# Performance work log

Hardware: AMD Instinct MI355X
Metric: run time of the kernel (lower is better)

## Reference

```python
import jax, jax.numpy as jnp
import numpy as np

H = 256   # input_size
P = 256   # state_size
BATCH, L = 8, 4096
DT_MIN, DT_MAX = 1e-3, 1e-1
LN_EPS = 1e-5


def _hippo_params():
    # HiPPO-N matrix (num_blocks=1), eigendecomposition in numpy (float64 then cast)
    idx = np.arange(P, dtype=np.float64)
    s = np.sqrt(idx + 0.5)
    A = -np.outer(s, s)
    A = np.tril(A) - np.triu(A, 1)
    np.fill_diagonal(A, -0.5)
    ev, V = np.linalg.eig(A)
    order = np.argsort(ev.real)
    ev, V = ev[order], V[:, order]
    return ev, V


def setup_inputs() -> dict:
    key = jax.random.key(0)
    k_u, = jax.random.split(key, 1)
    ev, V = _hippo_params()
    rng = np.random.default_rng(0)
    log_lambda_real = np.log(-np.clip(ev.real, None, -1e-4)).astype(np.float32)
    lambda_imag = ev.imag.astype(np.float32)
    V_inv = np.linalg.inv(V)
    B_init = rng.standard_normal((P, H)) / np.sqrt(P)
    B_tilde = V_inv @ B_init.astype(np.complex128)
    C_init = rng.standard_normal((H, P)) / np.sqrt(P)
    C_tilde = C_init.astype(np.complex128) @ V
    log_delta = (rng.random(P) * (np.log(DT_MAX) - np.log(DT_MIN)) + np.log(DT_MIN)).astype(np.float32)
    return {
        "u": jax.random.normal(k_u, (BATCH, L, H), dtype=jnp.float32),
        "log_lambda_real": jnp.asarray(log_lambda_real),
        "lambda_imag": jnp.asarray(lambda_imag),
        "B_tilde_real": jnp.asarray(B_tilde.real, dtype=jnp.float32),
        "B_tilde_imag": jnp.asarray(B_tilde.imag, dtype=jnp.float32),
        "C_tilde_real": jnp.asarray(C_tilde.real, dtype=jnp.float32),
        "C_tilde_imag": jnp.asarray(C_tilde.imag, dtype=jnp.float32),
        "log_delta": jnp.asarray(log_delta),
        "gamma": jnp.ones((H,), dtype=jnp.float32),
        "beta": jnp.zeros((H,), dtype=jnp.float32),
    }


def _layernorm(x, gamma, beta):
    mu = jnp.mean(x, axis=-1, keepdims=True)
    var = jnp.mean(jnp.square(x - mu), axis=-1, keepdims=True)
    return (x - mu) * jax.lax.rsqrt(var + LN_EPS) * gamma + beta


def _ssm(h, log_lambda_real, lambda_imag, B_tilde_real, B_tilde_imag,
         C_tilde_real, C_tilde_imag, log_delta):
    # Continuous-time diagonal SSM params
    lam = -jnp.exp(log_lambda_real) + 1j * lambda_imag            # (P,) complex
    B_tilde = B_tilde_real + 1j * B_tilde_imag                     # (P,H)
    C_tilde = C_tilde_real + 1j * C_tilde_imag                     # (H,P)
    delta = jnp.exp(log_delta)                                     # (P,)
    # ZOH discretization (eq. 6 of the S5 paper)
    lambda_bar = jnp.exp(lam * delta)                              # (P,)
    B_bar = ((lambda_bar - 1.0) / lam)[:, None] * B_tilde          # (P,H)
    # Bu_k = B_bar @ u_k  ->  (B,L,P) complex
    Bu = jnp.einsum('blh,ph->blp', h.astype(jnp.complex64), B_bar.astype(jnp.complex64))
    # Parallel associative scan for x_k = lambda_bar * x_{k-1} + Bu_k
    a = jnp.broadcast_to(lambda_bar.astype(jnp.complex64), Bu.shape)
    def combine(c1, c2):
        a1, b1 = c1
        a2, b2 = c2
        return a1 * a2, a2 * b1 + b2
    _, xs = jax.lax.associative_scan(combine, (a, Bu), axis=1)     # (B,L,P)
    # Project back to real output: y = Re(C_tilde @ x)
    y = jnp.einsum('blp,hp->blh', xs, C_tilde.astype(jnp.complex64)).real
    return y


def reference(u, log_lambda_real, lambda_imag, B_tilde_real, B_tilde_imag,
              C_tilde_real, C_tilde_imag, log_delta, gamma, beta):
    # S5Block: pre-LayerNorm -> S5 SSM -> GELU -> residual
    h = _layernorm(u, gamma, beta)
    y = _ssm(h, log_lambda_real, lambda_imag, B_tilde_real, B_tilde_imag,
             C_tilde_real, C_tilde_imag, log_delta)
    return u + jax.nn.gelu(y)
```

## Files before the change

### kernel.cpp

```cpp
#include <hip/hip_runtime.h>
#include <math.h>

#define HDIM 256
#define PDIM 256
#define BATCH 8
#define LSEQ 4096
#define MTOT (BATCH * LSEQ)
#define NCHUNK 128
#define CHLEN 32

typedef __attribute__((ext_vector_type(8))) short bf16x8;
typedef __attribute__((ext_vector_type(4))) float f32x4;

__device__ __forceinline__ unsigned short f2bf(float f) {
    union { float f; unsigned int u; } v; v.f = f;
    unsigned int r = v.u + 0x7FFFu + ((v.u >> 16) & 1u);
    return (unsigned short)(r >> 16);
}
__device__ __forceinline__ float bf2f(unsigned int lo16) {
    union { unsigned int u; float f; } v; v.u = lo16 << 16;
    return v.f;
}

__device__ __forceinline__ void gload_lds16(const void* g, void* l) {
    __builtin_amdgcn_global_load_lds(
        (const __attribute__((address_space(1))) void*)g,
        (__attribute__((address_space(3))) void*)l, 16, 0, 0);
}

__global__ void wpack_k(const float* __restrict__ llr, const float* __restrict__ lim,
                        const float* __restrict__ ldl,
                        const float* __restrict__ Br, const float* __restrict__ Bi,
                        const float* __restrict__ Cr, const float* __restrict__ Ci,
                        unsigned short* __restrict__ W1t, unsigned short* __restrict__ W2t,
                        float* __restrict__ par) {
    int h = threadIdx.x;
    if (blockIdx.x < PDIM) {
        int p = blockIdx.x;
        float er = expf(llr[p]);
        float im = lim[p];
        float d  = expf(ldl[p]);
        float zr = -er * d, zi = im * d;
        float ea = expf(zr);
        float sz, cz; sincosf(zi, &sz, &cz);
        float ar = ea * cz, ai = ea * sz;
        float dr = -er, di = im;
        float den = dr * dr + di * di;
        float nr = ar - 1.0f, ni = ai;
        float cr = (nr * dr + ni * di) / den;
        float ci = (ni * dr - nr * di) / den;
        float br = Br[p * HDIM + h], bi = Bi[p * HDIM + h];
        W1t[(2 * p) * HDIM + h]     = f2bf(cr * br - ci * bi);
        W1t[(2 * p + 1) * HDIM + h] = f2bf(cr * bi + ci * br);
    } else if (blockIdx.x < 2 * PDIM) {
        int p = blockIdx.x - PDIM;
        W2t[h * (2 * PDIM) + 2 * p]     = f2bf(Cr[h * PDIM + p]);
        W2t[h * (2 * PDIM) + 2 * p + 1] = f2bf(-Ci[h * PDIM + p]);
    } else {
        int p = h;
        float er = expf(llr[p]);
        float im = lim[p];
        float d  = expf(ldl[p]);
        float zr = -er * d, zi = im * d;
        float ea = expf(zr);
        float sz, cz; sincosf(zi, &sz, &cz);
        float ar = ea * cz, ai = ea * sz;
        float dr = -er, di = im;
        float den = dr * dr + di * di;
        float nr = ar - 1.0f, ni = ai;
        float cr = (nr * dr + ni * di) / den;
        float ci = (ni * dr - nr * di) / den;
        float eC = expf((float)CHLEN * zr);
        float sC, cC;
        sincosf((float)CHLEN * zi, &sC, &cC);
        par[2 * p]            = ar;
        par[2 * p + 1]        = ai;
        par[512 + 2 * p]      = cr;
        par[512 + 2 * p + 1]  = ci;
        par[1024 + 2 * p]     = eC * cC;
        par[1024 + 2 * p + 1] = eC * sC;
    }
}

__global__ void ln_k(const float* __restrict__ u, unsigned short* __restrict__ hbf,
                     const float* __restrict__ gamma, const float* __restrict__ beta) {
    __shared__ float gS[HDIM], bS[HDIM];
    int t = threadIdx.x;
    gS[t] = gamma[t]; bS[t] = beta[t];
    int lane = t & 63, wv = t >> 6;
    int row = blockIdx.x * 4 + wv;
    float4 v = *(const float4*)(u + (size_t)row * HDIM + lane * 4);
    float s  = v.x + v.y + v.z + v.w;
    float sq = v.x * v.x + v.y * v.y + v.z * v.z + v.w * v.w;
    #pragma unroll
    for (int o = 1; o < 64; o <<= 1) { s += __shfl_xor(s, o); sq += __shfl_xor(sq, o); }
    float mu = s * (1.0f / HDIM);
    float rs = rsqrtf(sq * (1.0f / HDIM) - mu * mu + 1e-5f);
    __syncthreads();
    int c = lane * 4;
    ushort4 o;
    o.x = f2bf((v.x - mu) * rs * gS[c + 0] + bS[c + 0]);
    o.y = f2bf((v.y - mu) * rs * gS[c + 1] + bS[c + 1]);
    o.z = f2bf((v.z - mu) * rs * gS[c + 2] + bS[c + 2]);
    o.w = f2bf((v.w - mu) * rs * gS[c + 3] + bS[c + 3]);
    *(ushort4*)(hbf + (size_t)row * HDIM + c) = o;
}

template <int MODE, int K>
__launch_bounds__(256, 2)
__global__ void mfma_gemm_k(const unsigned short* __restrict__ A,
                            const unsigned short* __restrict__ B,
                            void* __restrict__ outv,
                            const float* __restrict__ u,
                            int N) {
    __shared__ __align__(16) unsigned short As[2][128 * 32];
    __shared__ __align__(16) unsigned short Bs[2][128 * 32];
    const int t = threadIdx.x;

    const int nbn  = (int)gridDim.x;
    const int flat = (int)blockIdx.y * nbn + (int)blockIdx.x;
    const int nwg  = nbn * (int)gridDim.y;
    const int tile = (flat & 7) * (nwg >> 3) + (flat >> 3);
    const int bn = tile % nbn, bm = tile / nbn;

    const int lane = t & 63, w = t >> 6;

    const int srow   = 32 * w + (lane >> 2);
    const int schunk = (lane & 3) ^ ((lane >> 3) & 3);
    const unsigned short* gA = A + (size_t)(bm * 128 + srow) * K + schunk * 8;
    const unsigned short* gB = B + (size_t)(bn * 128 + srow) * K + schunk * 8;
    const int l0 = (32 * w) * 32;
    const int l1 = (32 * w + 16) * 32;

    const int wm = (w & 1) * 64;
    const int wn = (w >> 1) * 64;
    const int mrow = lane & 15;
    const int rsw  = (mrow >> 1) & 3;
    const int cch  = lane >> 4;
    const int fcol = ((cch ^ rsw) * 8);

    f32x4 acc[4][4] = {};
    constexpr int NT = K / 32;

    gload_lds16(gA,          &As[0][l0]);
    gload_lds16(gA + 16 * K, &As[0][l1]);
    gload_lds16(gB,          &Bs[0][l0]);
    gload_lds16(gB + 16 * K, &Bs[0][l1]);
    __syncthreads();

    #pragma unroll
    for (int tt = 0; tt < NT; ++tt) {
        const int cur = tt & 1;
        if (tt + 1 < NT) {
            const int k0 = (tt + 1) * 32;
            gload_lds16(gA + k0,          &As[cur ^ 1][l0]);
            gload_lds16(gA + 16 * K + k0, &As[cur ^ 1][l1]);
            gload_lds16(gB + k0,          &Bs[cur ^ 1][l0]);
            gload_lds16(gB + 16 * K + k0, &Bs[cur ^ 1][l1]);
        }
        bf16x8 fa[4], fb[4];
        #pragma unroll
        for (int i = 0; i < 4; i++) {
            fa[i] = *(const bf16x8*)&As[cur][(wm + i * 16 + mrow) * 32 + fcol];
            fb[i] = *(const bf16x8*)&Bs[cur][(wn + i * 16 + mrow) * 32 + fcol];
        }
        #pragma unroll
        for (int i = 0; i < 4; i++)
            #pragma unroll
            for (int j = 0; j < 4; j++)
                acc[i][j] = __builtin_amdgcn_mfma_f32_16x16x32_bf16(fa[i], fb[j], acc[i][j], 0, 0, 0);
        __syncthreads();
    }

    const int r0 = (lane >> 4) * 4;
    const int c0 = lane & 15;
    #pragma unroll
    for (int i = 0; i < 4; i++) {
        #pragma unroll
        for (int r = 0; r < 4; r++) {
            const size_t rowoff = (size_t)(bm * 128 + wm + i * 16 + r0 + r) * N;
            #pragma unroll
            for (int j = 0; j < 4; j++) {
                const int col_g = bn * 128 + wn + j * 16 + c0;
                float y = acc[i][j][r];
                if (MODE == 0) {
                    ((unsigned short*)outv)[rowoff + col_g] = f2bf(y);
                } else {
                    float z = 0.7978845608f * fmaf(0.044715f * y * y, y, y);
                    float e = __expf(2.0f * z);
                    float th = 1.0f - 2.0f / (e + 1.0f);
                    float g = 0.5f * y * (1.0f + th);
                    ((float*)outv)[rowoff + col_g] = u[rowoff + col_g] + g;
                }
            }
        }
    }
}

__global__ void scan_reduce_k(const unsigned short* __restrict__ Bu,
                              const float* __restrict__ par, float* __restrict__ last) {
    int t = threadIdx.x;
    int lane = t & 63, g = t >> 6;
    int c = blockIdx.x * 4 + g, b = blockIdx.y;
    int p0 = lane * 4;
    float4 a01 = *(const float4*)(par + 2 * p0);
    float4 a23 = *(const float4*)(par + 2 * p0 + 4);
    float ar[4] = {a01.x, a01.z, a23.x, a23.z};
    float ai[4] = {a01.y, a01.w, a23.y, a23.w};
    float xr[4] = {0.f, 0.f, 0.f, 0.f}, xi[4] = {0.f, 0.f, 0.f, 0.f};
    const uint4* q = (const uint4*)(Bu + ((size_t)b * LSEQ + (size_t)c * CHLEN) * 512) + lane;
    #pragma unroll 8
    for (int j = 0; j < CHLEN; j++) {
        uint4 v = q[(size_t)j * 64];
        unsigned int vv[4] = {v.x, v.y, v.z, v.w};
        #pragma unroll
        for (int k = 0; k < 4; k++) {
            float vr = bf2f(vv[k] & 0xFFFFu), vi = bf2f(vv[k] >> 16);
            float nr = fmaf(ar[k], xr[k], fmaf(-ai[k], xi[k], vr));
            float ni = fmaf(ar[k], xi[k], fmaf(ai[k], xr[k], vi));
            xr[k] = nr; xi[k] = ni;
        }
    }
    float* lp = last + ((size_t)b * NCHUNK + c) * 512 + 2 * p0;
    *(float4*)lp       = make_float4(xr[0], xi[0], xr[1], xi[1]);
    *(float4*)(lp + 4) = make_float4(xr[2], xi[2], xr[3], xi[3]);
}

__global__ void scan_carry_k(const float* __restrict__ last, float* __restrict__ prefix,
                             const float* __restrict__ par) {
    int p = threadIdx.x, b = blockIdx.x;
    float Ar = par[1024 + 2 * p], Ai = par[1024 + 2 * p + 1];
    float Pr = 0.0f, Pi = 0.0f;
    const float2* lp = (const float2*)(last + (size_t)b * NCHUNK * 512) + p;
    float2* pp = (float2*)(prefix + (size_t)b * NCHUNK * 512) + p;
    for (int c0 = 0; c0 < NCHUNK; c0 += 16) {
        float2 v[16];
        #pragma unroll
        for (int j = 0; j < 16; j++) v[j] = lp[(size_t)(c0 + j) * 256];
        #pragma unroll
        for (int j = 0; j < 16; j++) {
            pp[(size_t)(c0 + j) * 256] = make_float2(Pr, Pi);
            float nr = fmaf(Ar, Pr, fmaf(-Ai, Pi, v[j].x));
            float ni = fmaf(Ar, Pi, fmaf(Ai, Pr, v[j].y));
            Pr = nr; Pi = ni;
        }
    }
}

__global__ void scan_apply_k(unsigned short* __restrict__ Bu, const float* __restrict__ par,
                             const float* __restrict__ prefix) {
    int t = threadIdx.x;
    int lane = t & 63, g = t >> 6;
    int c = blockIdx.x * 4 + g, b = blockIdx.y;
    int p0 = lane * 4;
    float4 a01 = *(const float4*)(par + 2 * p0);
    float4 a23 = *(const float4*)(par + 2 * p0 + 4);
    float ar[4] = {a01.x, a01.z, a23.x, a23.z};
    float ai[4] = {a01.y, a01.w, a23.y, a23.w};
    const float* pf = prefix + ((size_t)b * NCHUNK + c) * 512 + 2 * p0;
    float4 P01 = *(const float4*)pf;
    float4 P23 = *(const float4*)(pf + 4);
    float xr[4] = {P01.x, P01.z, P23.x, P23.z};
    float xi[4] = {P01.y, P01.w, P23.y, P23.w};
    uint4* q = (uint4*)(Bu + ((size_t)b * LSEQ + (size_t)c * CHLEN) * 512) + lane;
    #pragma unroll 8
    for (int j = 0; j < CHLEN; j++) {
        uint4 v = q[(size_t)j * 64];
        unsigned int vv[4] = {v.x, v.y, v.z, v.w};
        #pragma unroll
        for (int k = 0; k < 4; k++) {
            float vr = bf2f(vv[k] & 0xFFFFu), vi = bf2f(vv[k] >> 16);
            float nr = fmaf(ar[k], xr[k], fmaf(-ai[k], xi[k], vr));
            float ni = fmaf(ar[k], xi[k], fmaf(ai[k], xr[k], vi));
            xr[k] = nr; xi[k] = ni;
            vv[k] = (unsigned int)f2bf(nr) | ((unsigned int)f2bf(ni) << 16);
        }
        uint4 o; o.x = vv[0]; o.y = vv[1]; o.z = vv[2]; o.w = vv[3];
        q[(size_t)j * 64] = o;
    }
}

extern "C" void kernel_launch(void* const* d_in, const int* in_sizes, int n_in,
                              void* d_out, int out_size, void* d_ws, size_t ws_size,
                              hipStream_t stream) {
    const float* u   = (const float*)d_in[0];
    const float* llr = (const float*)d_in[1];
    const float* lim = (const float*)d_in[2];
    const float* Br  = (const float*)d_in[3];
    const float* Bi  = (const float*)d_in[4];
    const float* Cr  = (const float*)d_in[5];
    const float* Ci  = (const float*)d_in[6];
    const float* ldl = (const float*)d_in[7];
    const float* gam = (const float*)d_in[8];
    const float* bet = (const float*)d_in[9];
    float* out = (float*)d_out;

    float* ws     = (float*)d_ws;
    float* par    = ws;
    float* last   = ws + 2048;
    float* prefix = last + (size_t)BATCH * NCHUNK * 512;
    unsigned short* W1t = (unsigned short*)(prefix + (size_t)BATCH * NCHUNK * 512);
    unsigned short* W2t = W1t + 512 * HDIM;
    unsigned short* hbf = W2t + HDIM * 512;
    unsigned short* Bu  = hbf + (size_t)MTOT * HDIM;

    ln_k<<<MTOT / 4, 256, 0, stream>>>(u, hbf, gam, bet);
    wpack_k<<<2 * PDIM + 1, HDIM, 0, stream>>>(llr, lim, ldl, Br, Bi, Cr, Ci, W1t, W2t, par);

    mfma_gemm_k<0, HDIM><<<dim3(512 / 128, MTOT / 128), 256, 0, stream>>>(
        hbf, W1t, (void*)Bu, nullptr, 512);

    scan_reduce_k<<<dim3(NCHUNK / 4, BATCH), 256, 0, stream>>>(Bu, par, last);
    scan_carry_k<<<BATCH, PDIM, 0, stream>>>(last, prefix, par);
    scan_apply_k<<<dim3(NCHUNK / 4, BATCH), 256, 0, stream>>>(Bu, par, prefix);

    mfma_gemm_k<1, 512><<<dim3(HDIM / 128, MTOT / 128), 256, 0, stream>>>(
        Bu, W2t, (void*)out, u, HDIM);
}
```

Baseline: 168.4 us.

## Fuse LayerNorm into first GEMM and scan-apply into second GEMM

LayerNorm is now computed directly into a full 128x256 bf16 LDS tile inside the first GEMM, so the normalized activation buffer is no longer written to or read from global memory. The scan-apply step is moved into the second GEMM: each block rebuilds the 32-row chunk of scanned states in LDS from the chunk prefix and then multiplies it against the full 256-column output projection, which removes the Bu write-back and reread and drops two launches. In exchange, the first GEMM recomputes LayerNorm once for each of its 4 column blocks, LDS use rises (a 64KB A tile), and the second GEMM runs with smaller 32-row M tiles and lower occupancy.

Result: slower. 178.9 us (+6.2%).

```diff
diff --git a/kernel.cpp b/kernel.cpp
--- a/kernel.cpp
+++ b/kernel.cpp
@@ -82,40 +82,14 @@
     }
 }
 
-__global__ void ln_k(const float* __restrict__ u, unsigned short* __restrict__ hbf,
-                     const float* __restrict__ gamma, const float* __restrict__ beta) {
-    __shared__ float gS[HDIM], bS[HDIM];
-    int t = threadIdx.x;
-    gS[t] = gamma[t]; bS[t] = beta[t];
-    int lane = t & 63, wv = t >> 6;
-    int row = blockIdx.x * 4 + wv;
-    float4 v = *(const float4*)(u + (size_t)row * HDIM + lane * 4);
-    float s  = v.x + v.y + v.z + v.w;
-    float sq = v.x * v.x + v.y * v.y + v.z * v.z + v.w * v.w;
-    #pragma unroll
-    for (int o = 1; o < 64; o <<= 1) { s += __shfl_xor(s, o); sq += __shfl_xor(sq, o); }
-    float mu = s * (1.0f / HDIM);
-    float rs = rsqrtf(sq * (1.0f / HDIM) - mu * mu + 1e-5f);
-    __syncthreads();
-    int c = lane * 4;
-    ushort4 o;
-    o.x = f2bf((v.x - mu) * rs * gS[c + 0] + bS[c + 0]);
-    o.y = f2bf((v.y - mu) * rs * gS[c + 1] + bS[c + 1]);
-    o.z = f2bf((v.z - mu) * rs * gS[c + 2] + bS[c + 2]);
-    o.w = f2bf((v.w - mu) * rs * gS[c + 3] + bS[c + 3]);
-    *(ushort4*)(hbf + (size_t)row * HDIM + c) = o;
-}
-
-template <int MODE, int K>
 __launch_bounds__(256, 2)
-__global__ void mfma_gemm_k(const unsigned short* __restrict__ A,
-                            const unsigned short* __restrict__ B,
-                            void* __restrict__ outv,
-                            const float* __restrict__ u,
-                            int N) {
-    __shared__ __align__(16) unsigned short As[2][128 * 32];
+__global__ void ln_gemm1_k(const float* __restrict__ u, const unsigned short* __restrict__ W1t,
+                           unsigned short* __restrict__ Bu,
+                           const float* __restrict__ gamma, const float* __restrict__ beta) {
+    __shared__ __align__(16) unsigned short As[128 * 256];
     __shared__ __align__(16) unsigned short Bs[2][128 * 32];
     const int t = threadIdx.x;
+    const int lane = t & 63, w = t >> 6;
 
     const int nbn  = (int)gridDim.x;
     const int flat = (int)blockIdx.y * nbn + (int)blockIdx.x;
@@ -123,29 +97,45 @@
     const int tile = (flat & 7) * (nwg >> 3) + (flat >> 3);
     const int bn = tile % nbn, bm = tile / nbn;
 
-    const int lane = t & 63, w = t >> 6;
-
     const int srow   = 32 * w + (lane >> 2);
     const int schunk = (lane & 3) ^ ((lane >> 3) & 3);
-    const unsigned short* gA = A + (size_t)(bm * 128 + srow) * K + schunk * 8;
-    const unsigned short* gB = B + (size_t)(bn * 128 + srow) * K + schunk * 8;
-    const int l0 = (32 * w) * 32;
-    const int l1 = (32 * w + 16) * 32;
-
-    const int wm = (w & 1) * 64;
-    const int wn = (w >> 1) * 64;
+    const unsigned short* gB = W1t + (size_t)(bn * 128 + srow) * HDIM + schunk * 8;
+    const int bl0 = (32 * w) * 32;
+    const int bl1 = (32 * w + 16) * 32;
+
+    gload_lds16(gB,             &Bs[0][bl0]);
+    gload_lds16(gB + 16 * HDIM, &Bs[0][bl1]);
+
+    const float4 g4 = *(const float4*)(gamma + lane * 4);
+    const float4 b4 = *(const float4*)(beta + lane * 4);
+    #pragma unroll 4
+    for (int i = 0; i < 32; i++) {
+        const int row = i * 4 + w;
+        const float4 v = *(const float4*)(u + (size_t)(bm * 128 + row) * HDIM + lane * 4);
+        float s  = v.x + v.y + v.z + v.w;
+        float sq = v.x * v.x + v.y * v.y + v.z * v.z + v.w * v.w;
+        #pragma unroll
+        for (int o = 1; o < 64; o <<= 1) { s += __shfl_xor(s, o); sq += __shfl_xor(sq, o); }
+        const float mu = s * (1.0f / HDIM);
+        const float rs = rsqrtf(sq * (1.0f / HDIM) - mu * mu + 1e-5f);
+        ushort4 o4;
+        o4.x = f2bf((v.x - mu) * rs * g4.x + b4.x);
+        o4.y = f2bf((v.y - mu) * rs * g4.y + b4.y);
+        o4.z = f2bf((v.z - mu) * rs * g4.z + b4.z);
+        o4.w = f2bf((v.w - mu) * rs * g4.w + b4.w);
+        const int idx = row * 256 + ((((lane >> 1) ^ (row & 7)) << 3) + (lane & 1) * 4);
+        *(ushort4*)&As[idx] = o4;
+    }
+
+    const int wm = (w & 1) * 64, wn = (w >> 1) * 64;
     const int mrow = lane & 15;
     const int rsw  = (mrow >> 1) & 3;
     const int cch  = lane >> 4;
-    const int fcol = ((cch ^ rsw) * 8);
+    const int fcol = (cch ^ rsw) * 8;
 
     f32x4 acc[4][4] = {};
-    constexpr int NT = K / 32;
-
-    gload_lds16(gA,          &As[0][l0]);
-    gload_lds16(gA + 16 * K, &As[0][l1]);
-    gload_lds16(gB,          &Bs[0][l0]);
-    gload_lds16(gB + 16 * K, &Bs[0][l1]);
+    constexpr int NT = HDIM / 32;
+
     __syncthreads();
 
     #pragma unroll
@@ -153,15 +143,15 @@
         const int cur = tt & 1;
         if (tt + 1 < NT) {
             const int k0 = (tt + 1) * 32;
-            gload_lds16(gA + k0,          &As[cur ^ 1][l0]);
-            gload_lds16(gA + 16 * K + k0, &As[cur ^ 1][l1]);
-            gload_lds16(gB + k0,          &Bs[cur ^ 1][l0]);
-            gload_lds16(gB + 16 * K + k0, &Bs[cur ^ 1][l1]);
-        }
+            gload_lds16(gB + k0,             &Bs[cur ^ 1][bl0]);
+            gload_lds16(gB + 16 * HDIM + k0, &Bs[cur ^ 1][bl1]);
+        }
+        const int cb = tt * 4;
         bf16x8 fa[4], fb[4];
         #pragma unroll
         for (int i = 0; i < 4; i++) {
-            fa[i] = *(const bf16x8*)&As[cur][(wm + i * 16 + mrow) * 32 + fcol];
+            const int r = wm + i * 16 + mrow;
+            fa[i] = *(const bf16x8*)&As[r * 256 + (((cb + cch) ^ (r & 7)) << 3)];
             fb[i] = *(const bf16x8*)&Bs[cur][(wn + i * 16 + mrow) * 32 + fcol];
         }
         #pragma unroll
@@ -172,27 +162,15 @@
         __syncthreads();
     }
 
-    const int r0 = (lane >> 4) * 4;
-    const int c0 = lane & 15;
+    const int r0 = (lane >> 4) * 4, c0 = lane & 15;
     #pragma unroll
     for (int i = 0; i < 4; i++) {
         #pragma unroll
         for (int r = 0; r < 4; r++) {
-            const size_t rowoff = (size_t)(bm * 128 + wm + i * 16 + r0 + r) * N;
-            #pragma unroll
-            for (int j = 0; j < 4; j++) {
-                const int col_g = bn * 128 + wn + j * 16 + c0;
-                float y = acc[i][j][r];
-                if (MODE == 0) {
-                    ((unsigned short*)outv)[rowoff + col_g] = f2bf(y);
-                } else {
-                    float z = 0.7978845608f * fmaf(0.044715f * y * y, y, y);
-                    float e = __expf(2.0f * z);
-                    float th = 1.0f - 2.0f / (e + 1.0f);
-                    float g = 0.5f * y * (1.0f + th);
-                    ((float*)outv)[rowoff + col_g] = u[rowoff + col_g] + g;
-                }
-            }
+            const size_t rowoff = (size_t)(bm * 128 + wm + i * 16 + r0 + r) * 512;
+            #pragma unroll
+            for (int j = 0; j < 4; j++)
+                Bu[rowoff + bn * 128 + wn + j * 16 + c0] = f2bf(acc[i][j][r]);
         }
     }
 }
@@ -247,36 +225,102 @@
     }
 }
 
-__global__ void scan_apply_k(unsigned short* __restrict__ Bu, const float* __restrict__ par,
-                             const float* __restrict__ prefix) {
-    int t = threadIdx.x;
-    int lane = t & 63, g = t >> 6;
-    int c = blockIdx.x * 4 + g, b = blockIdx.y;
-    int p0 = lane * 4;
-    float4 a01 = *(const float4*)(par + 2 * p0);
-    float4 a23 = *(const float4*)(par + 2 * p0 + 4);
-    float ar[4] = {a01.x, a01.z, a23.x, a23.z};
-    float ai[4] = {a01.y, a01.w, a23.y, a23.w};
-    const float* pf = prefix + ((size_t)b * NCHUNK + c) * 512 + 2 * p0;
-    float4 P01 = *(const float4*)pf;
-    float4 P23 = *(const float4*)(pf + 4);
-    float xr[4] = {P01.x, P01.z, P23.x, P23.z};
-    float xi[4] = {P01.y, P01.w, P23.y, P23.w};
-    uint4* q = (uint4*)(Bu + ((size_t)b * LSEQ + (size_t)c * CHLEN) * 512) + lane;
-    #pragma unroll 8
-    for (int j = 0; j < CHLEN; j++) {
-        uint4 v = q[(size_t)j * 64];
-        unsigned int vv[4] = {v.x, v.y, v.z, v.w};
-        #pragma unroll
-        for (int k = 0; k < 4; k++) {
-            float vr = bf2f(vv[k] & 0xFFFFu), vi = bf2f(vv[k] >> 16);
-            float nr = fmaf(ar[k], xr[k], fmaf(-ai[k], xi[k], vr));
-            float ni = fmaf(ar[k], xi[k], fmaf(ai[k], xr[k], vi));
-            xr[k] = nr; xi[k] = ni;
-            vv[k] = (unsigned int)f2bf(nr) | ((unsigned int)f2bf(ni) << 16);
-        }
-        uint4 o; o.x = vv[0]; o.y = vv[1]; o.z = vv[2]; o.w = vv[3];
-        q[(size_t)j * 64] = o;
+__launch_bounds__(256, 2)
+__global__ void apply_gemm2_k(const unsigned short* __restrict__ Bu,
+                              const float* __restrict__ par,
+                              const float* __restrict__ prefix,
+                              const unsigned short* __restrict__ W2t,
+                              const float* __restrict__ u, float* __restrict__ out) {
+    __shared__ __align__(16) unsigned short Xs[32 * 512];
+    __shared__ __align__(16) unsigned short Bs[2][256 * 32];
+    const int t = threadIdx.x;
+    const int lane = t & 63, w = t >> 6;
+    const int c = blockIdx.x, b = blockIdx.y;
+    const size_t row0 = (size_t)b * LSEQ + (size_t)c * CHLEN;
+
+    const int srow   = 64 * w + (lane >> 2);
+    const int schunk = (lane & 3) ^ ((lane >> 3) & 3);
+    const unsigned short* gB = W2t + (size_t)srow * 512 + schunk * 8;
+    const int bl0 = (64 * w) * 32;
+
+    #pragma unroll
+    for (int m = 0; m < 4; m++)
+        gload_lds16(gB + m * 16 * 512, &Bs[0][bl0 + m * 16 * 32]);
+
+    {
+        const int p = t;
+        const unsigned int* q = (const unsigned int*)(Bu + row0 * 512) + p;
+        unsigned int vv[32];
+        #pragma unroll
+        for (int j = 0; j < 32; j++) vv[j] = q[(size_t)j * 256];
+        const float2 P = ((const float2*)(prefix + ((size_t)b * NCHUNK + c) * 512))[p];
+        const float ar = par[2 * p], ai = par[2 * p + 1];
+        float xr = P.x, xi = P.y;
+        #pragma unroll
+        for (int j = 0; j < 32; j++) {
+            float vr = bf2f(vv[j] & 0xFFFFu), vi = bf2f(vv[j] >> 16);
+            float nr = fmaf(ar, xr, fmaf(-ai, xi, vr));
+            float ni = fmaf(ar, xi, fmaf(ai, xr, vi));
+            xr = nr; xi = ni;
+            unsigned int pk = (unsigned int)f2bf(xr) | ((unsigned int)f2bf(xi) << 16);
+            *(unsigned int*)&Xs[j * 512 + ((((p >> 2) ^ (j & 7)) << 3) + (p & 3) * 2)] = pk;
+        }
+    }
+
+    const int mrow = lane & 15;
+    const int rsw  = (mrow >> 1) & 3;
+    const int cch  = lane >> 4;
+    const int fcol = (cch ^ rsw) * 8;
+
+    f32x4 acc[2][4] = {};
+    constexpr int NT = 16;
+
+    __syncthreads();
+
+    #pragma unroll
+    for (int tt = 0; tt < NT; ++tt) {
+        const int cur = tt & 1;
+        if (tt + 1 < NT) {
+            const int k0 = (tt + 1) * 32;
+            #pragma unroll
+            for (int m = 0; m < 4; m++)
+                gload_lds16(gB + m * 16 * 512 + k0, &Bs[cur ^ 1][bl0 + m * 16 * 32]);
+        }
+        const int cb = tt * 4;
+        bf16x8 fa[2], fb[4];
+        #pragma unroll
+        for (int i = 0; i < 2; i++) {
+            const int r = i * 16 + mrow;
+            fa[i] = *(const bf16x8*)&Xs[r * 512 + (((cb + cch) ^ (r & 7)) << 3)];
+        }
+        #pragma unroll
+        for (int j = 0; j < 4; j++)
+            fb[j] = *(const bf16x8*)&Bs[cur][(64 * w + j * 16 + mrow) * 32 + fcol];
+        #pragma unroll
+        for (int i = 0; i < 2; i++)
+            #pragma unroll
+            for (int j = 0; j < 4; j++)
+                acc[i][j] = __builtin_amdgcn_mfma_f32_16x16x32_bf16(fa[i], fb[j], acc[i][j], 0, 0, 0);
+        __syncthreads();
+    }
+
+    const int r0 = (lane >> 4) * 4, c0 = lane & 15;
+    #pragma unroll
+    for (int i = 0; i < 2; i++) {
+        #pragma unroll
+        for (int r = 0; r < 4; r++) {
+            const size_t rowoff = (row0 + i * 16 + r0 + r) * HDIM;
+            #pragma unroll
+            for (int j = 0; j < 4; j++) {
+                const int col = 64 * w + j * 16 + c0;
+                float y = acc[i][j][r];
+                float z = 0.7978845608f * fmaf(0.044715f * y * y, y, y);
+                float e = __expf(2.0f * z);
+                float th = 1.0f - 2.0f / (e + 1.0f);
+                float g = 0.5f * y * (1.0f + th);
+                out[rowoff + col] = u[rowoff + col] + g;
+            }
+        }
     }
 }
 
@@ -301,19 +345,14 @@
     float* prefix = last + (size_t)BATCH * NCHUNK * 512;
     unsigned short* W1t = (unsigned short*)(prefix + (size_t)BATCH * NCHUNK * 512);
     unsigned short* W2t = W1t + 512 * HDIM;
-    unsigned short* hbf = W2t + HDIM * 512;
-    unsigned short* Bu  = hbf + (size_t)MTOT * HDIM;
-
-    ln_k<<<MTOT / 4, 256, 0, stream>>>(u, hbf, gam, bet);
+    unsigned short* Bu  = W2t + HDIM * 512;
+
     wpack_k<<<2 * PDIM + 1, HDIM, 0, stream>>>(llr, lim, ldl, Br, Bi, Cr, Ci, W1t, W2t, par);
 
-    mfma_gemm_k<0, HDIM><<<dim3(512 / 128, MTOT / 128), 256, 0, stream>>>(
-        hbf, W1t, (void*)Bu, nullptr, 512);
+    ln_gemm1_k<<<dim3(512 / 128, MTOT / 128), 256, 0, stream>>>(u, W1t, Bu, gam, bet);
 
     scan_reduce_k<<<dim3(NCHUNK / 4, BATCH), 256, 0, stream>>>(Bu, par, last);
     scan_carry_k<<<BATCH, PDIM, 0, stream>>>(last, prefix, par);
-    scan_apply_k<<<dim3(NCHUNK / 4, BATCH), 256, 0, stream>>>(Bu, par, prefix);
-
-    mfma_gemm_k<1, 512><<<dim3(HDIM / 128, MTOT / 128), 256, 0, stream>>>(
-        Bu, W2t, (void*)out, u, HDIM);
-}
+
+    apply_gemm2_k<<<dim3(NCHUNK, BATCH), 256, 0, stream>>>(Bu, par, prefix, W2t, u, out);
+}
```

## Keep full weight panel in LDS and stream A fragments from global into registers

Applied to the files above, without the earlier changes.

Replaces the shared double-buffered LDS GEMM with two specialized kernels. Each block loads its whole weight slice (full K) into swizzled LDS once and streams the activation fragments straight from global memory into registers, with a one-step register prefetch. Blocks grow to 512 threads over 256-row M tiles, and the per-k-step __syncthreads barriers go away. The cost is 64 KB of LDS per block, which caps occupancy, and uncoalesced direct global fragment loads that the L2 cache has to absorb.

After: 206.7 us. 22.8% more time.

```diff
diff --git a/kernel.cpp b/kernel.cpp
--- a/kernel.cpp
+++ b/kernel.cpp
@@ -20,12 +20,6 @@
 __device__ __forceinline__ float bf2f(unsigned int lo16) {
     union { unsigned int u; float f; } v; v.u = lo16 << 16;
     return v.f;
-}
-
-__device__ __forceinline__ void gload_lds16(const void* g, void* l) {
-    __builtin_amdgcn_global_load_lds(
-        (const __attribute__((address_space(1))) void*)g,
-        (__attribute__((address_space(3))) void*)l, 16, 0, 0);
 }
 
 __global__ void wpack_k(const float* __restrict__ llr, const float* __restrict__ lim,
@@ -106,16 +100,13 @@
     *(ushort4*)(hbf + (size_t)row * HDIM + c) = o;
 }
 
-template <int MODE, int K>
-__launch_bounds__(256, 2)
-__global__ void mfma_gemm_k(const unsigned short* __restrict__ A,
-                            const unsigned short* __restrict__ B,
-                            void* __restrict__ outv,
-                            const float* __restrict__ u,
-                            int N) {
-    __shared__ __align__(16) unsigned short As[2][128 * 32];
-    __shared__ __align__(16) unsigned short Bs[2][128 * 32];
+__launch_bounds__(512, 4)
+__global__ void gemm1_k(const unsigned short* __restrict__ A,
+                        const unsigned short* __restrict__ W1t,
+                        unsigned short* __restrict__ Bu) {
+    __shared__ __align__(16) unsigned short Bs[128 * 256];
     const int t = threadIdx.x;
+    const int lane = t & 63, w = t >> 6;
 
     const int nbn  = (int)gridDim.x;
     const int flat = (int)blockIdx.y * nbn + (int)blockIdx.x;
@@ -123,75 +114,132 @@
     const int tile = (flat & 7) * (nwg >> 3) + (flat >> 3);
     const int bn = tile % nbn, bm = tile / nbn;
 
-    const int lane = t & 63, w = t >> 6;
-
-    const int srow   = 32 * w + (lane >> 2);
-    const int schunk = (lane & 3) ^ ((lane >> 3) & 3);
-    const unsigned short* gA = A + (size_t)(bm * 128 + srow) * K + schunk * 8;
-    const unsigned short* gB = B + (size_t)(bn * 128 + srow) * K + schunk * 8;
-    const int l0 = (32 * w) * 32;
-    const int l1 = (32 * w + 16) * 32;
-
-    const int wm = (w & 1) * 64;
-    const int wn = (w >> 1) * 64;
-    const int mrow = lane & 15;
-    const int rsw  = (mrow >> 1) & 3;
-    const int cch  = lane >> 4;
-    const int fcol = ((cch ^ rsw) * 8);
+    #pragma unroll
+    for (int k = 0; k < 8; k++) {
+        const int ci = t * 8 + k;
+        const int n = ci >> 5, c = ci & 31;
+        uint4 v = *(const uint4*)(W1t + (size_t)(bn * 128 + n) * HDIM + c * 8);
+        *(uint4*)&Bs[n * 256 + ((c ^ (n & 7)) * 8)] = v;
+    }
+
+    const int wm = (w >> 1) * 64, wn = (w & 1) * 64;
+    const int mrow = lane & 15, cch = lane >> 4;
+    const unsigned short* gA = A + (size_t)(bm * 256 + wm + mrow) * HDIM + cch * 8;
+
+    bf16x8 fa[4];
+    #pragma unroll
+    for (int i = 0; i < 4; i++) fa[i] = *(const bf16x8*)(gA + i * 16 * HDIM);
 
     f32x4 acc[4][4] = {};
-    constexpr int NT = K / 32;
-
-    gload_lds16(gA,          &As[0][l0]);
-    gload_lds16(gA + 16 * K, &As[0][l1]);
-    gload_lds16(gB,          &Bs[0][l0]);
-    gload_lds16(gB + 16 * K, &Bs[0][l1]);
     __syncthreads();
 
     #pragma unroll
-    for (int tt = 0; tt < NT; ++tt) {
-        const int cur = tt & 1;
-        if (tt + 1 < NT) {
-            const int k0 = (tt + 1) * 32;
-            gload_lds16(gA + k0,          &As[cur ^ 1][l0]);
-            gload_lds16(gA + 16 * K + k0, &As[cur ^ 1][l1]);
-            gload_lds16(gB + k0,          &Bs[cur ^ 1][l0]);
-            gload_lds16(gB + 16 * K + k0, &Bs[cur ^ 1][l1]);
-        }
-        bf16x8 fa[4], fb[4];
-        #pragma unroll
-        for (int i = 0; i < 4; i++) {
-            fa[i] = *(const bf16x8*)&As[cur][(wm + i * 16 + mrow) * 32 + fcol];
-            fb[i] = *(const bf16x8*)&Bs[cur][(wn + i * 16 + mrow) * 32 + fcol];
+    for (int tt = 0; tt < HDIM / 32; tt++) {
+        bf16x8 fnext[4];
+        if (tt + 1 < HDIM / 32) {
+            #pragma unroll
+            for (int i = 0; i < 4; i++)
+                fnext[i] = *(const bf16x8*)(gA + i * 16 * HDIM + (tt + 1) * 32);
+        }
+        bf16x8 fb[4];
+        #pragma unroll
+        for (int j = 0; j < 4; j++) {
+            const int n = wn + j * 16 + mrow;
+            fb[j] = *(const bf16x8*)&Bs[n * 256 + (((tt * 4 + cch) ^ (n & 7)) * 8)];
         }
         #pragma unroll
         for (int i = 0; i < 4; i++)
             #pragma unroll
             for (int j = 0; j < 4; j++)
                 acc[i][j] = __builtin_amdgcn_mfma_f32_16x16x32_bf16(fa[i], fb[j], acc[i][j], 0, 0, 0);
-        __syncthreads();
-    }
-
-    const int r0 = (lane >> 4) * 4;
-    const int c0 = lane & 15;
+        #pragma unroll
+        for (int i = 0; i < 4; i++) fa[i] = fnext[i];
+    }
+
+    const int r0 = (lane >> 4) * 4, c0 = lane & 15;
     #pragma unroll
     for (int i = 0; i < 4; i++) {
         #pragma unroll
         for (int r = 0; r < 4; r++) {
-            const size_t rowoff = (size_t)(bm * 128 + wm + i * 16 + r0 + r) * N;
-            #pragma unroll
-            for (int j = 0; j < 4; j++) {
-                const int col_g = bn * 128 + wn + j * 16 + c0;
+            const size_t rowoff = (size_t)(bm * 256 + wm + i * 16 + r0 + r) * 512;
+            #pragma unroll
+            for (int j = 0; j < 4; j++)
+                Bu[rowoff + bn * 128 + wn + j * 16 + c0] = f2bf(acc[i][j][r]);
+        }
+    }
+}
+
+__launch_bounds__(512, 4)
+__global__ void gemm2_k(const unsigned short* __restrict__ X,
+                        const unsigned short* __restrict__ W2t,
+                        const float* __restrict__ u, float* __restrict__ out) {
+    __shared__ __align__(16) unsigned short Bs[64 * 512];
+    const int t = threadIdx.x;
+    const int lane = t & 63, w = t >> 6;
+
+    const int nbn  = (int)gridDim.x;
+    const int flat = (int)blockIdx.y * nbn + (int)blockIdx.x;
+    const int nwg  = nbn * (int)gridDim.y;
+    const int tile = (flat & 7) * (nwg >> 3) + (flat >> 3);
+    const int bn = tile % nbn, bm = tile / nbn;
+
+    #pragma unroll
+    for (int k = 0; k < 8; k++) {
+        const int ci = t * 8 + k;
+        const int n = ci >> 6, c = ci & 63;
+        uint4 v = *(const uint4*)(W2t + (size_t)(bn * 64 + n) * 512 + c * 8);
+        *(uint4*)&Bs[n * 512 + ((c ^ (n & 7)) * 8)] = v;
+    }
+
+    const int wm = (w >> 1) * 64, wn = (w & 1) * 32;
+    const int mrow = lane & 15, cch = lane >> 4;
+    const unsigned short* gA = X + (size_t)(bm * 256 + wm + mrow) * 512 + cch * 8;
+
+    bf16x8 fa[4];
+    #pragma unroll
+    for (int i = 0; i < 4; i++) fa[i] = *(const bf16x8*)(gA + i * 16 * 512);
+
+    f32x4 acc[4][2] = {};
+    __syncthreads();
+
+    #pragma unroll
+    for (int tt = 0; tt < 16; tt++) {
+        bf16x8 fnext[4];
+        if (tt + 1 < 16) {
+            #pragma unroll
+            for (int i = 0; i < 4; i++)
+                fnext[i] = *(const bf16x8*)(gA + i * 16 * 512 + (tt + 1) * 32);
+        }
+        bf16x8 fb[2];
+        #pragma unroll
+        for (int j = 0; j < 2; j++) {
+            const int n = wn + j * 16 + mrow;
+            fb[j] = *(const bf16x8*)&Bs[n * 512 + (((tt * 4 + cch) ^ (n & 7)) * 8)];
+        }
+        #pragma unroll
+        for (int i = 0; i < 4; i++)
+            #pragma unroll
+            for (int j = 0; j < 2; j++)
+                acc[i][j] = __builtin_amdgcn_mfma_f32_16x16x32_bf16(fa[i], fb[j], acc[i][j], 0, 0, 0);
+        #pragma unroll
+        for (int i = 0; i < 4; i++) fa[i] = fnext[i];
+    }
+
+    const int r0 = (lane >> 4) * 4, c0 = lane & 15;
+    #pragma unroll
+    for (int i = 0; i < 4; i++) {
+        #pragma unroll
+        for (int r = 0; r < 4; r++) {
+            const size_t rowoff = (size_t)(bm * 256 + wm + i * 16 + r0 + r) * HDIM;
+            #pragma unroll
+            for (int j = 0; j < 2; j++) {
+                const int col = bn * 64 + wn + j * 16 + c0;
                 float y = acc[i][j][r];
-                if (MODE == 0) {
-                    ((unsigned short*)outv)[rowoff + col_g] = f2bf(y);
-                } else {
-                    float z = 0.7978845608f * fmaf(0.044715f * y * y, y, y);
-                    float e = __expf(2.0f * z);
-                    float th = 1.0f - 2.0f / (e + 1.0f);
-                    float g = 0.5f * y * (1.0f + th);
-                    ((float*)outv)[rowoff + col_g] = u[rowoff + col_g] + g;
-                }
+                float z = 0.7978845608f * fmaf(0.044715f * y * y, y, y);
+                float e = __expf(2.0f * z);
+                float th = 1.0f - 2.0f / (e + 1.0f);
+                float g = 0.5f * y * (1.0f + th);
+                out[rowoff + col] = u[rowoff + col] + g;
             }
         }
     }
@@ -307,13 +355,11 @@
     ln_k<<<MTOT / 4, 256, 0, stream>>>(u, hbf, gam, bet);
     wpack_k<<<2 * PDIM + 1, HDIM, 0, stream>>>(llr, lim, ldl, Br, Bi, Cr, Ci, W1t, W2t, par);
 
-    mfma_gemm_k<0, HDIM><<<dim3(512 / 128, MTOT / 128), 256, 0, stream>>>(
-        hbf, W1t, (void*)Bu, nullptr, 512);
+    gemm1_k<<<dim3(4, MTOT / 256), 512, 0, stream>>>(hbf, W1t, Bu);
 
     scan_reduce_k<<<dim3(NCHUNK / 4, BATCH), 256, 0, stream>>>(Bu, par, last);
     scan_carry_k<<<BATCH, PDIM, 0, stream>>>(last, prefix, par);
     scan_apply_k<<<dim3(NCHUNK / 4, BATCH), 256, 0, stream>>>(Bu, par, prefix);
 
-    mfma_gemm_k<1, 512><<<dim3(HDIM / 128, MTOT / 128), 256, 0, stream>>>(
-        Bu, W2t, (void*)out, u, HDIM);
-}
+    gemm2_k<<<dim3(4, MTOT / 256), 512, 0, stream>>>(Bu, W2t, u, out);
+}
```
